# Optimization experiments

Hardware: AMD Instinct MI355X
Metric: run time of the kernel (lower is better)

Reference implementation:

```python
import jax, jax.numpy as jnp
import numpy as np

D = 64
H = 2          # n_heads
HD = D // H    # head_dim = 32
EPS = 1e-5


def _layer_norm(x, gamma, beta):
    mu = jnp.mean(x, axis=-1, keepdims=True)
    var = jnp.var(x, axis=-1, keepdims=True)
    return (x - mu) * jax.lax.rsqrt(var + EPS) * gamma + beta


def setup_inputs() -> dict:
    key = jax.random.key(0)
    ks = jax.random.split(key, 12)
    s = 0.05
    n_stocks, tau = 512, 512
    return {
        "x":     jax.random.normal(ks[0], (n_stocks, tau, D), dtype=jnp.float32),
        "Wqkv":  jax.random.normal(ks[1], (3 * D, D), dtype=jnp.float32) * s,
        "bqkv":  jax.random.normal(ks[2], (3 * D,), dtype=jnp.float32) * s,
        "Wo":    jax.random.normal(ks[3], (D, D), dtype=jnp.float32) * s,
        "bo":    jax.random.normal(ks[4], (D,), dtype=jnp.float32) * s,
        "g1":    jnp.ones((D,), dtype=jnp.float32),
        "beta1": jnp.zeros((D,), dtype=jnp.float32),
        "W1":    jax.random.normal(ks[5], (4 * D, D), dtype=jnp.float32) * s,
        "bf1":   jax.random.normal(ks[6], (4 * D,), dtype=jnp.float32) * s,
        "W2":    jax.random.normal(ks[7], (D, 4 * D), dtype=jnp.float32) * s,
        "bf2":   jax.random.normal(ks[8], (D,), dtype=jnp.float32) * s,
        "g2":    jnp.ones((D,), dtype=jnp.float32),
        "beta2": jnp.zeros((D,), dtype=jnp.float32),
    }


def reference(x, Wqkv, bqkv, Wo, bo, g1, beta1, W1, bf1, W2, bf2, g2, beta2):
    # x: (n_stocks, tau, D). The torch loop over tau == batched attention with
    # batch = tau, seq = n_stocks. Dropout is identity (eval mode).
    n_stocks, tau, d = x.shape
    Ht = jnp.transpose(x, (1, 0, 2))                    # (tau, S, D)

    qkv = Ht @ Wqkv.T + bqkv                            # (tau, S, 3D)
    q, k, v = jnp.split(qkv, 3, axis=-1)
    q = q.reshape(tau, n_stocks, H, HD)
    k = k.reshape(tau, n_stocks, H, HD)
    v = v.reshape(tau, n_stocks, H, HD)

    scores = jnp.einsum("bqhd,bkhd->bhqk", q, k) / jnp.sqrt(jnp.float32(HD))
    attn = jax.nn.softmax(scores, axis=-1)              # (tau, H, S, S)
    ctx = jnp.einsum("bhqk,bkhd->bqhd", attn, v).reshape(tau, n_stocks, D)
    attn_out = ctx @ Wo.T + bo                          # (tau, S, D)

    y = _layer_norm(attn_out + Ht, g1, beta1)           # residual + LN1
    ffn = jax.nn.relu(y @ W1.T + bf1) @ W2.T + bf2      # (tau, S, D)
    z = _layer_norm(ffn + y, g2, beta2)                 # residual + LN2

    return jnp.transpose(z, (1, 0, 2))                  # (n_stocks, tau, D)
```

## Files before the change

### kernel.cpp

```cpp
#include <hip/hip_runtime.h>
#include <hip/hip_bf16.h>
#include <cmath>

#define NS 512
#define NT 512
#define DIM 64
#define HD 32

typedef __attribute__((ext_vector_type(8))) short short8;
typedef __attribute__((ext_vector_type(16))) float f32x16;

union FragU { unsigned w[4]; short8 f; };

__device__ __forceinline__ unsigned short bfbits(float x) {
  __hip_bfloat16 h = __float2bfloat16(x);
  return __builtin_bit_cast(unsigned short, h);
}
__device__ __forceinline__ unsigned pk2(float lo, float hi) {
  return (unsigned)bfbits(lo) | ((unsigned)bfbits(hi) << 16);
}
__device__ __forceinline__ float lo_f(unsigned w) { return __uint_as_float(w << 16); }
__device__ __forceinline__ float hi_f(unsigned w) { return __uint_as_float(w & 0xffff0000u); }
__device__ __forceinline__ short8 ldg8(const __hip_bfloat16* p) {
  return *reinterpret_cast<const short8*>(p);
}

__device__ __forceinline__ void repack(const float* p, int hi, short8& o1, short8& o2) {
  unsigned pk[8], xk[8];
  #pragma unroll
  for (int j = 0; j < 8; ++j) pk[j] = pk2(p[2 * j], p[2 * j + 1]);
  #pragma unroll
  for (int j = 0; j < 8; ++j) xk[j] = (unsigned)__shfl_xor((int)pk[j], 32, 64);
  FragU a1, a2;
  a1.w[0] = hi ? xk[2] : pk[0];
  a1.w[1] = hi ? xk[3] : pk[1];
  a1.w[2] = hi ? pk[2] : xk[0];
  a1.w[3] = hi ? pk[3] : xk[1];
  a2.w[0] = hi ? xk[6] : pk[4];
  a2.w[1] = hi ? xk[7] : pk[5];
  a2.w[2] = hi ? pk[6] : xk[4];
  a2.w[3] = hi ? pk[7] : xk[5];
  o1 = a1.f; o2 = a2.f;
}

__global__ void k_cvt(const float* __restrict__ Wqkv, const float* __restrict__ Wo,
                      const float* __restrict__ W1, const float* __restrict__ W2,
                      __hip_bfloat16* __restrict__ dst) {
  int i = blockIdx.x * 256 + threadIdx.x;
  float v;
  if (i < 12288) v = Wqkv[i];
  else if (i < 16384) v = Wo[i - 12288];
  else if (i < 32768) v = W1[i - 16384];
  else v = W2[i - 32768];
  dst[i] = __float2bfloat16(v);
}

__global__ __launch_bounds__(512, 4) void k_attn(
    const float* __restrict__ x, const __hip_bfloat16* __restrict__ Wb,
    const float* __restrict__ bqkv, __hip_bfloat16* __restrict__ ctx) {
  __shared__ char smem[65536];
  const int t = blockIdx.x, h = blockIdx.y;
  const int tid = threadIdx.x;
  const int l = tid & 63, wv = tid >> 6, hi = l >> 5, l31 = l & 31;

  {
    const float4* xp = reinterpret_cast<const float4*>(x + ((size_t)tid * NT + t) * DIM);
    unsigned xpk[32];
    #pragma unroll
    for (int i = 0; i < 16; ++i) {
      float4 v = xp[i];
      xpk[2 * i]     = pk2(v.x, v.y);
      xpk[2 * i + 1] = pk2(v.z, v.w);
    }
    #pragma unroll
    for (int c = 0; c < 8; ++c) {
      FragU fu;
      fu.w[0] = xpk[4*c]; fu.w[1] = xpk[4*c+1]; fu.w[2] = xpk[4*c+2]; fu.w[3] = xpk[4*c+3];
      *reinterpret_cast<short8*>(smem + tid * 128 + ((c ^ (tid & 7)) << 4)) = fu.f;
    }
  }
  __syncthreads();

  short8 xf[2][4];
  #pragma unroll
  for (int rt = 0; rt < 2; ++rt) {
    int row = wv * 64 + rt * 32 + l31;
    #pragma unroll
    for (int st = 0; st < 4; ++st)
      xf[rt][st] = *reinterpret_cast<const short8*>(
          smem + row * 128 + ((((st << 1) | hi) ^ (row & 7)) << 4));
  }
  __syncthreads();

  short8 qfrag[2][2];
  {
    short8 wqa[4];
    #pragma unroll
    for (int st = 0; st < 4; ++st)
      wqa[st] = ldg8(Wb + (size_t)(h * 32 + l31) * 64 + st * 16 + hi * 8);
    float bqv[16];
    #pragma unroll
    for (int r = 0; r < 16; ++r)
      bqv[r] = bqkv[h * 32 + (r & 3) + 8 * (r >> 2) + 4 * hi];
    #pragma unroll
    for (int rt = 0; rt < 2; ++rt) {
      f32x16 qa = {};
      #pragma unroll
      for (int st = 0; st < 4; ++st)
        qa = __builtin_amdgcn_mfma_f32_32x32x16_bf16(wqa[st], xf[rt][st], qa, 0, 0, 0);
      float p[16];
      #pragma unroll
      for (int r = 0; r < 16; ++r) p[r] = (qa[r] + bqv[r]) * 0.17677669529663687f;
      repack(p, hi, qfrag[rt][0], qfrag[rt][1]);
    }
  }

  {
    short8 wkb[4];
    #pragma unroll
    for (int st = 0; st < 4; ++st)
      wkb[st] = ldg8(Wb + (size_t)(64 + h * 32 + l31) * 64 + st * 16 + hi * 8);
    float bk = bqkv[64 + h * 32 + l31];
    #pragma unroll
    for (int rt = 0; rt < 2; ++rt) {
      f32x16 ka = {};
      #pragma unroll
      for (int st = 0; st < 4; ++st)
        ka = __builtin_amdgcn_mfma_f32_32x32x16_bf16(xf[rt][st], wkb[st], ka, 0, 0, 0);
      #pragma unroll
      for (int r = 0; r < 16; ++r) {
        int key = wv * 64 + rt * 32 + (r & 3) + 8 * (r >> 2) + 4 * hi;
        *reinterpret_cast<unsigned short*>(
            smem + key * 64 + (((l31 >> 3) ^ (key & 3)) << 4) + ((l31 & 7) << 1)) =
            bfbits(ka[r] + bk);
      }
    }
  }

  {
    short8 wvb[4];
    #pragma unroll
    for (int st = 0; st < 4; ++st)
      wvb[st] = ldg8(Wb + (size_t)(128 + h * 32 + l31) * 64 + st * 16 + hi * 8);
    float bv = bqkv[128 + h * 32 + l31];
    #pragma unroll
    for (int rt = 0; rt < 2; ++rt) {
      f32x16 va = {};
      #pragma unroll
      for (int st = 0; st < 4; ++st)
        va = __builtin_amdgcn_mfma_f32_32x32x16_bf16(xf[rt][st], wvb[st], va, 0, 0, 0);
      #pragma unroll
      for (int g = 0; g < 4; ++g) {
        int kb = wv * 64 + rt * 32 + g * 8 + hi * 4;
        uint2 d2 = make_uint2(pk2(va[4*g] + bv, va[4*g+1] + bv),
                              pk2(va[4*g+2] + bv, va[4*g+3] + bv));
        *reinterpret_cast<uint2*>(
            smem + 32768 + l31 * 1024 + ((((kb >> 3) ^ (l31 & 7)) << 4) + ((kb & 7) << 1))) = d2;
      }
    }
  }
  __syncthreads();

  f32x16 oacc[2];
  #pragma unroll
  for (int i = 0; i < 16; ++i) { oacc[0][i] = 0.f; oacc[1][i] = 0.f; }
  float lsum[2] = {0.f, 0.f};

  #pragma clang loop unroll(disable)
  for (int kt = 0; kt < 16; ++kt) {
    short8 kfrag[2], vfrag[2];
    #pragma unroll
    for (int dc = 0; dc < 2; ++dc) {
      int row = kt * 32 + l31;
      kfrag[dc] = *reinterpret_cast<const short8*>(
          smem + row * 64 + ((((dc << 1) | hi) ^ (l31 & 3)) << 4));
    }
    #pragma unroll
    for (int c = 0; c < 2; ++c) {
      int ck = kt * 4 + (c << 1) + hi;
      vfrag[c] = *reinterpret_cast<const short8*>(
          smem + 32768 + l31 * 1024 + ((ck ^ (l31 & 7)) << 4));
    }
    #pragma unroll
    for (int sb = 0; sb < 2; ++sb) {
      f32x16 st = {};
      st = __builtin_amdgcn_mfma_f32_32x32x16_bf16(kfrag[0], qfrag[sb][0], st, 0, 0, 0);
      st = __builtin_amdgcn_mfma_f32_32x32x16_bf16(kfrag[1], qfrag[sb][1], st, 0, 0, 0);
      float p[16];
      #pragma unroll
      for (int r = 0; r < 16; ++r) { p[r] = __expf(st[r]); lsum[sb] += p[r]; }
      short8 a1, a2;
      repack(p, hi, a1, a2);
      oacc[sb] = __builtin_amdgcn_mfma_f32_32x32x16_bf16(a1, vfrag[0], oacc[sb], 0, 0, 0);
      oacc[sb] = __builtin_amdgcn_mfma_f32_32x32x16_bf16(a2, vfrag[1], oacc[sb], 0, 0, 0);
    }
  }

  #pragma unroll
  for (int sb = 0; sb < 2; ++sb) {
    float lt = lsum[sb] + __shfl_xor(lsum[sb], 32, 64);
    float inv = 1.f / lt;
    #pragma unroll
    for (int r = 0; r < 16; ++r) {
      int ql = (r & 3) + 8 * (r >> 2) + 4 * hi;
      float fac = __shfl(inv, ql, 64);
      int q = wv * 64 + sb * 32 + ql;
      ctx[((size_t)t * 512 + q) * 64 + h * 32 + l31] = __float2bfloat16(oacc[sb][r] * fac);
    }
  }
}

__global__ __launch_bounds__(512, 2) void k_tail(
    const __hip_bfloat16* __restrict__ ctx, const float* __restrict__ x,
    const __hip_bfloat16* __restrict__ Wob, const float* __restrict__ bo,
    const float* __restrict__ g1, const float* __restrict__ be1,
    const __hip_bfloat16* __restrict__ W1b, const float* __restrict__ bf1,
    const __hip_bfloat16* __restrict__ W2b, const float* __restrict__ bf2,
    const float* __restrict__ g2, const float* __restrict__ be2,
    float* __restrict__ out) {
  __shared__ char sm[133632];
  float* ps = reinterpret_cast<float*>(sm + 131072);
  const int t = blockIdx.x;
  const int tid = threadIdx.x;
  const int l = tid & 63, wv = tid >> 6, hi = l >> 5, l31 = l & 31;

  {
    const short8* cp = reinterpret_cast<const short8*>(ctx + ((size_t)t * 512 + tid) * 64);
    #pragma unroll
    for (int c = 0; c < 8; ++c)
      *reinterpret_cast<short8*>(sm + tid * 128 + ((c ^ (tid & 7)) << 4)) = cp[c];
  }
  for (int i = tid; i < 640; i += 512) {
    float v;
    if (i < 64) v = g1[i];
    else if (i < 128) v = be1[i - 64];
    else if (i < 192) v = bo[i - 128];
    else if (i < 256) v = bf2[i - 192];
    else if (i < 320) v = g2[i - 256];
    else if (i < 384) v = be2[i - 320];
    else v = bf1[i - 384];
    ps[i] = v;
  }
  __syncthreads();

  {
    short8 cb[2][4];
    #pragma unroll
    for (int stl = 0; stl < 2; ++stl) {
      int row = wv * 64 + stl * 32 + l31;
      #pragma unroll
      for (int st = 0; st < 4; ++st)
        cb[stl][st] = *reinterpret_cast<const short8*>(
            sm + row * 128 + ((((st << 1) | hi) ^ (row & 7)) << 4));
    }
    f32x16 ao[2][2];
    #pragma unroll
    for (int dt = 0; dt < 2; ++dt) {
      short8 wa[4];
      #pragma unroll
      for (int st = 0; st < 4; ++st)
        wa[st] = ldg8(Wob + (size_t)(dt * 32 + l31) * 64 + st * 16 + hi * 8);
      #pragma unroll
      for (int stl = 0; stl < 2; ++stl) {
        f32x16 a = {};
        #pragma unroll
        for (int st = 0; st < 4; ++st)
          a = __builtin_amdgcn_mfma_f32_32x32x16_bf16(wa[st], cb[stl][st], a, 0, 0, 0);
        ao[dt][stl] = a;
      }
    }
    #pragma unroll
    for (int dt = 0; dt < 2; ++dt)
      #pragma unroll
      for (int stl = 0; stl < 2; ++stl) {
        int s_ = wv * 64 + stl * 32 + l31;
        #pragma unroll
        for (int rp = 0; rp < 8; ++rp) {
          int r = 2 * rp;
          int d = dt * 32 + (r & 3) + 8 * (r >> 2) + 4 * hi;
          *reinterpret_cast<unsigned*>(
              sm + s_ * 128 + (((d >> 3) ^ (s_ & 7)) << 4) + ((d & 7) << 1)) =
              pk2(ao[dt][stl][r], ao[dt][stl][r + 1]);
        }
      }
  }
  __syncthreads();

  float y[64];
  {
    float aov[64];
    #pragma unroll
    for (int c = 0; c < 8; ++c) {
      FragU fu;
      fu.f = *reinterpret_cast<const short8*>(sm + tid * 128 + ((c ^ (tid & 7)) << 4));
      #pragma unroll
      for (int u = 0; u < 4; ++u) {
        aov[c * 8 + 2 * u]     = lo_f(fu.w[u]);
        aov[c * 8 + 2 * u + 1] = hi_f(fu.w[u]);
      }
    }
    const float4* xp = reinterpret_cast<const float4*>(x + ((size_t)tid * NT + t) * DIM);
    #pragma unroll
    for (int i = 0; i < 16; ++i) {
      float4 v = xp[i];
      y[4*i+0] = v.x + aov[4*i+0] + ps[128 + 4*i+0];
      y[4*i+1] = v.y + aov[4*i+1] + ps[128 + 4*i+1];
      y[4*i+2] = v.z + aov[4*i+2] + ps[128 + 4*i+2];
      y[4*i+3] = v.w + aov[4*i+3] + ps[128 + 4*i+3];
    }
    float m0 = 0.f, m1 = 0.f, m2 = 0.f, m3 = 0.f;
    #pragma unroll
    for (int j = 0; j < 16; ++j) {
      m0 += y[4*j+0]; m1 += y[4*j+1]; m2 += y[4*j+2]; m3 += y[4*j+3];
    }
    float mu = ((m0 + m1) + (m2 + m3)) * (1.f / 64.f);
    float v0 = 0.f, v1 = 0.f, v2 = 0.f, v3 = 0.f;
    #pragma unroll
    for (int j = 0; j < 16; ++j) {
      float t0 = y[4*j+0] - mu, t1 = y[4*j+1] - mu;
      float t2 = y[4*j+2] - mu, t3 = y[4*j+3] - mu;
      v0 = fmaf(t0, t0, v0); v1 = fmaf(t1, t1, v1);
      v2 = fmaf(t2, t2, v2); v3 = fmaf(t3, t3, v3);
    }
    float var = ((v0 + v1) + (v2 + v3)) * (1.f / 64.f);
    float rs = rsqrtf(var + 1e-5f);
    #pragma unroll
    for (int d = 0; d < 64; ++d) y[d] = (y[d] - mu) * rs * ps[d] + ps[64 + d];
    #pragma unroll
    for (int c = 0; c < 8; ++c) {
      FragU fu;
      #pragma unroll
      for (int u = 0; u < 4; ++u) fu.w[u] = pk2(y[c*8 + 2*u], y[c*8 + 2*u + 1]);
      *reinterpret_cast<short8*>(sm + 65536 + tid * 128 + ((c ^ (tid & 7)) << 4)) = fu.f;
    }
  }
  __syncthreads();

  {
    short8 yb[2][4];
    #pragma unroll
    for (int stl = 0; stl < 2; ++stl) {
      int row = wv * 64 + stl * 32 + l31;
      #pragma unroll
      for (int st = 0; st < 4; ++st)
        yb[stl][st] = *reinterpret_cast<const short8*>(
            sm + 65536 + row * 128 + ((((st << 1) | hi) ^ (row & 7)) << 4));
    }
    f32x16 zacc[2][2];
    #pragma unroll
    for (int i = 0; i < 16; ++i) {
      zacc[0][0][i] = 0.f; zacc[0][1][i] = 0.f; zacc[1][0][i] = 0.f; zacc[1][1][i] = 0.f;
    }
    #pragma clang loop unroll(disable)
    for (int jt = 0; jt < 8; ++jt) {
      short8 w1a[4];
      #pragma unroll
      for (int st = 0; st < 4; ++st)
        w1a[st] = ldg8(W1b + (size_t)(jt * 32 + l31) * 64 + st * 16 + hi * 8);
      short8 w2f[2][2];
      #pragma unroll
      for (int dt = 0; dt < 2; ++dt)
        #pragma unroll
        for (int ks = 0; ks < 2; ++ks)
          w2f[dt][ks] = ldg8(W2b + (size_t)(dt * 32 + l31) * 256 + jt * 32 + ks * 16 + hi * 8);
      float b1v[16];
      #pragma unroll
      for (int r = 0; r < 16; ++r)
        b1v[r] = ps[384 + jt * 32 + (r & 3) + 8 * (r >> 2) + 4 * hi];
      #pragma unroll
      for (int stl = 0; stl < 2; ++stl) {
        f32x16 ha = {};
        #pragma unroll
        for (int st = 0; st < 4; ++st)
          ha = __builtin_amdgcn_mfma_f32_32x32x16_bf16(w1a[st], yb[stl][st], ha, 0, 0, 0);
        float p[16];
        #pragma unroll
        for (int r = 0; r < 16; ++r) p[r] = fmaxf(ha[r] + b1v[r], 0.f);
        short8 b1, b2;
        repack(p, hi, b1, b2);
        zacc[0][stl] = __builtin_amdgcn_mfma_f32_32x32x16_bf16(w2f[0][0], b1, zacc[0][stl], 0, 0, 0);
        zacc[0][stl] = __builtin_amdgcn_mfma_f32_32x32x16_bf16(w2f[0][1], b2, zacc[0][stl], 0, 0, 0);
        zacc[1][stl] = __builtin_amdgcn_mfma_f32_32x32x16_bf16(w2f[1][0], b1, zacc[1][stl], 0, 0, 0);
        zacc[1][stl] = __builtin_amdgcn_mfma_f32_32x32x16_bf16(w2f[1][1], b2, zacc[1][stl], 0, 0, 0);
      }
    }
    #pragma unroll
    for (int dt = 0; dt < 2; ++dt)
      #pragma unroll
      for (int stl = 0; stl < 2; ++stl) {
        int s_ = wv * 64 + stl * 32 + l31;
        #pragma unroll
        for (int rp = 0; rp < 8; ++rp) {
          int r = 2 * rp;
          int d = dt * 32 + (r & 3) + 8 * (r >> 2) + 4 * hi;
          *reinterpret_cast<unsigned*>(
              sm + s_ * 128 + (((d >> 3) ^ (s_ & 7)) << 4) + ((d & 7) << 1)) =
              pk2(zacc[dt][stl][r], zacc[dt][stl][r + 1]);
        }
      }
  }
  __syncthreads();

  {
    float z[64];
    #pragma unroll
    for (int c = 0; c < 8; ++c) {
      FragU zf, yf;
      zf.f = *reinterpret_cast<const short8*>(sm + tid * 128 + ((c ^ (tid & 7)) << 4));
      yf.f = *reinterpret_cast<const short8*>(sm + 65536 + tid * 128 + ((c ^ (tid & 7)) << 4));
      #pragma unroll
      for (int u = 0; u < 4; ++u) {
        int d = c * 8 + 2 * u;
        z[d]     = lo_f(zf.w[u]) + ps[192 + d]     + lo_f(yf.w[u]);
        z[d + 1] = hi_f(zf.w[u]) + ps[192 + d + 1] + hi_f(yf.w[u]);
      }
    }
    float m0 = 0.f, m1 = 0.f, m2 = 0.f, m3 = 0.f;
    #pragma unroll
    for (int j = 0; j < 16; ++j) {
      m0 += z[4*j+0]; m1 += z[4*j+1]; m2 += z[4*j+2]; m3 += z[4*j+3];
    }
    float mu2 = ((m0 + m1) + (m2 + m3)) * (1.f / 64.f);
    float v0 = 0.f, v1 = 0.f, v2 = 0.f, v3 = 0.f;
    #pragma unroll
    for (int j = 0; j < 16; ++j) {
      float t0 = z[4*j+0] - mu2, t1 = z[4*j+1] - mu2;
      float t2 = z[4*j+2] - mu2, t3 = z[4*j+3] - mu2;
      v0 = fmaf(t0, t0, v0); v1 = fmaf(t1, t1, v1);
      v2 = fmaf(t2, t2, v2); v3 = fmaf(t3, t3, v3);
    }
    float var2 = ((v0 + v1) + (v2 + v3)) * (1.f / 64.f);
    float rs2 = rsqrtf(var2 + 1e-5f);
    float4* op = reinterpret_cast<float4*>(out + ((size_t)tid * NT + t) * DIM);
    #pragma unroll
    for (int i = 0; i < 16; ++i) {
      op[i] = make_float4(
          (z[4*i+0] - mu2) * rs2 * ps[256 + 4*i+0] + ps[320 + 4*i+0],
          (z[4*i+1] - mu2) * rs2 * ps[256 + 4*i+1] + ps[320 + 4*i+1],
          (z[4*i+2] - mu2) * rs2 * ps[256 + 4*i+2] + ps[320 + 4*i+2],
          (z[4*i+3] - mu2) * rs2 * ps[256 + 4*i+3] + ps[320 + 4*i+3]);
    }
  }
}

extern "C" void kernel_launch(void* const* d_in, const int* in_sizes, int n_in,
                              void* d_out, int out_size, void* d_ws, size_t ws_size,
                              hipStream_t stream) {
  const float* x    = (const float*)d_in[0];
  const float* Wqkv = (const float*)d_in[1];
  const float* bqkv = (const float*)d_in[2];
  const float* Wo   = (const float*)d_in[3];
  const float* bo   = (const float*)d_in[4];
  const float* g1   = (const float*)d_in[5];
  const float* be1  = (const float*)d_in[6];
  const float* W1   = (const float*)d_in[7];
  const float* bf1  = (const float*)d_in[8];
  const float* W2   = (const float*)d_in[9];
  const float* bf2  = (const float*)d_in[10];
  const float* g2   = (const float*)d_in[11];
  const float* be2  = (const float*)d_in[12];
  float* out = (float*)d_out;

  __hip_bfloat16* wb   = (__hip_bfloat16*)d_ws;
  __hip_bfloat16* ctxb = (__hip_bfloat16*)((char*)d_ws + 131072);

  hipLaunchKernelGGL(k_cvt, dim3(192), dim3(256), 0, stream, Wqkv, Wo, W1, W2, wb);
  hipLaunchKernelGGL(k_attn, dim3(NT, 2), dim3(512), 0, stream, x, wb, bqkv, ctxb);
  hipLaunchKernelGGL(k_tail, dim3(NT), dim3(512), 0, stream,
                     ctxb, x, wb + 12288, bo, g1, be1, wb + 16384, bf1,
                     wb + 32768, bf2, g2, be2, out);
}
```

Baseline: 173.9 us.

## Rework attention and tail kernels: direct x loads, permlane repack, exp2, smaller tail blocks

k_attn now builds its x fragments straight from global memory, which removes an LDS staging pass and two barriers. It replaces shuffle-based repacking with v_permlane32_swap and folds log2(e) into the Q scale so it can use exp2. The K bias is dropped, since it shifts every score of a query by the same amount and cancels in the softmax, and the V bias is applied once at the ctx write. k_tail is split into 256-thread blocks over two stock halves with far less shared memory, keeps y in registers, and writes through transposed MFMA outputs, removing barriers and raising occupancy. The main risks are wave-local LDS reuse without barriers and the changed fragment layouts.

```diff
diff --git a/kernel.cpp b/kernel.cpp
--- a/kernel.cpp
+++ b/kernel.cpp
@@ -12,6 +12,12 @@
 
 union FragU { unsigned w[4]; short8 f; };
 
+#if __has_builtin(__builtin_amdgcn_exp2f)
+#define EXP2F __builtin_amdgcn_exp2f
+#else
+#define EXP2F exp2f
+#endif
+
 __device__ __forceinline__ unsigned short bfbits(float x) {
   __hip_bfloat16 h = __float2bfloat16(x);
   return __builtin_bit_cast(unsigned short, h);
@@ -25,21 +31,21 @@
   return *reinterpret_cast<const short8*>(p);
 }
 
-__device__ __forceinline__ void repack(const float* p, int hi, short8& o1, short8& o2) {
-  unsigned pk[8], xk[8];
+__device__ __forceinline__ void pl32swap(unsigned& a, unsigned& b) {
+  asm volatile("v_permlane32_swap_b32 %0, %1" : "+v"(a), "+v"(b));
+}
+
+__device__ __forceinline__ void repack(const float* p, short8& o1, short8& o2) {
+  unsigned pk[8];
   #pragma unroll
   for (int j = 0; j < 8; ++j) pk[j] = pk2(p[2 * j], p[2 * j + 1]);
-  #pragma unroll
-  for (int j = 0; j < 8; ++j) xk[j] = (unsigned)__shfl_xor((int)pk[j], 32, 64);
+  pl32swap(pk[0], pk[2]);
+  pl32swap(pk[1], pk[3]);
+  pl32swap(pk[4], pk[6]);
+  pl32swap(pk[5], pk[7]);
   FragU a1, a2;
-  a1.w[0] = hi ? xk[2] : pk[0];
-  a1.w[1] = hi ? xk[3] : pk[1];
-  a1.w[2] = hi ? pk[2] : xk[0];
-  a1.w[3] = hi ? pk[3] : xk[1];
-  a2.w[0] = hi ? xk[6] : pk[4];
-  a2.w[1] = hi ? xk[7] : pk[5];
-  a2.w[2] = hi ? pk[6] : xk[4];
-  a2.w[3] = hi ? pk[7] : xk[5];
+  a1.w[0] = pk[0]; a1.w[1] = pk[1]; a1.w[2] = pk[2]; a1.w[3] = pk[3];
+  a2.w[0] = pk[4]; a2.w[1] = pk[5]; a2.w[2] = pk[6]; a2.w[3] = pk[7];
   o1 = a1.f; o2 = a2.f;
 }
 
@@ -63,34 +69,65 @@
   const int tid = threadIdx.x;
   const int l = tid & 63, wv = tid >> 6, hi = l >> 5, l31 = l & 31;
 
-  {
-    const float4* xp = reinterpret_cast<const float4*>(x + ((size_t)tid * NT + t) * DIM);
-    unsigned xpk[32];
-    #pragma unroll
-    for (int i = 0; i < 16; ++i) {
-      float4 v = xp[i];
-      xpk[2 * i]     = pk2(v.x, v.y);
-      xpk[2 * i + 1] = pk2(v.z, v.w);
-    }
-    #pragma unroll
-    for (int c = 0; c < 8; ++c) {
-      FragU fu;
-      fu.w[0] = xpk[4*c]; fu.w[1] = xpk[4*c+1]; fu.w[2] = xpk[4*c+2]; fu.w[3] = xpk[4*c+3];
-      *reinterpret_cast<short8*>(smem + tid * 128 + ((c ^ (tid & 7)) << 4)) = fu.f;
-    }
-  }
-  __syncthreads();
-
   short8 xf[2][4];
   #pragma unroll
   for (int rt = 0; rt < 2; ++rt) {
     int row = wv * 64 + rt * 32 + l31;
+    const float* xr = x + ((size_t)row * NT + t) * DIM + hi * 8;
+    #pragma unroll
+    for (int st = 0; st < 4; ++st) {
+      float4 f0 = *reinterpret_cast<const float4*>(xr + st * 16);
+      float4 f1 = *reinterpret_cast<const float4*>(xr + st * 16 + 4);
+      FragU fu;
+      fu.w[0] = pk2(f0.x, f0.y); fu.w[1] = pk2(f0.z, f0.w);
+      fu.w[2] = pk2(f1.x, f1.y); fu.w[3] = pk2(f1.z, f1.w);
+      xf[rt][st] = fu.f;
+    }
+  }
+
+  {
+    short8 wkb[4];
     #pragma unroll
     for (int st = 0; st < 4; ++st)
-      xf[rt][st] = *reinterpret_cast<const short8*>(
-          smem + row * 128 + ((((st << 1) | hi) ^ (row & 7)) << 4));
-  }
-  __syncthreads();
+      wkb[st] = ldg8(Wb + (size_t)(64 + h * 32 + l31) * 64 + st * 16 + hi * 8);
+    #pragma unroll
+    for (int rt = 0; rt < 2; ++rt) {
+      f32x16 ka = {};
+      #pragma unroll
+      for (int st = 0; st < 4; ++st)
+        ka = __builtin_amdgcn_mfma_f32_32x32x16_bf16(wkb[st], xf[rt][st], ka, 0, 0, 0);
+      int stock = wv * 64 + rt * 32 + l31;
+      char* kb = smem + stock * 64 + (hi << 3);
+      #pragma unroll
+      for (int rq = 0; rq < 4; ++rq) {
+        uint2 d2 = make_uint2(pk2(ka[4 * rq + 0], ka[4 * rq + 1]),
+                              pk2(ka[4 * rq + 2], ka[4 * rq + 3]));
+        *reinterpret_cast<uint2*>(kb + ((rq ^ ((stock >> 1) & 3)) << 4)) = d2;
+      }
+    }
+  }
+
+  {
+    short8 wvb[4];
+    #pragma unroll
+    for (int st = 0; st < 4; ++st)
+      wvb[st] = ldg8(Wb + (size_t)(128 + h * 32 + l31) * 64 + st * 16 + hi * 8);
+    #pragma unroll
+    for (int rt = 0; rt < 2; ++rt) {
+      f32x16 va = {};
+      #pragma unroll
+      for (int st = 0; st < 4; ++st)
+        va = __builtin_amdgcn_mfma_f32_32x32x16_bf16(xf[rt][st], wvb[st], va, 0, 0, 0);
+      #pragma unroll
+      for (int g = 0; g < 4; ++g) {
+        int kb = wv * 64 + rt * 32 + g * 8 + hi * 4;
+        uint2 d2 = make_uint2(pk2(va[4 * g + 0], va[4 * g + 1]),
+                              pk2(va[4 * g + 2], va[4 * g + 3]));
+        *reinterpret_cast<uint2*>(
+            smem + 32768 + l31 * 1024 + (((kb >> 3) ^ (l31 & 7)) << 4) + ((kb & 7) << 1)) = d2;
+      }
+    }
+  }
 
   short8 qfrag[2][2];
   {
@@ -110,55 +147,16 @@
         qa = __builtin_amdgcn_mfma_f32_32x32x16_bf16(wqa[st], xf[rt][st], qa, 0, 0, 0);
       float p[16];
       #pragma unroll
-      for (int r = 0; r < 16; ++r) p[r] = (qa[r] + bqv[r]) * 0.17677669529663687f;
-      repack(p, hi, qfrag[rt][0], qfrag[rt][1]);
-    }
-  }
-
-  {
-    short8 wkb[4];
-    #pragma unroll
-    for (int st = 0; st < 4; ++st)
-      wkb[st] = ldg8(Wb + (size_t)(64 + h * 32 + l31) * 64 + st * 16 + hi * 8);
-    float bk = bqkv[64 + h * 32 + l31];
-    #pragma unroll
-    for (int rt = 0; rt < 2; ++rt) {
-      f32x16 ka = {};
-      #pragma unroll
-      for (int st = 0; st < 4; ++st)
-        ka = __builtin_amdgcn_mfma_f32_32x32x16_bf16(xf[rt][st], wkb[st], ka, 0, 0, 0);
-      #pragma unroll
-      for (int r = 0; r < 16; ++r) {
-        int key = wv * 64 + rt * 32 + (r & 3) + 8 * (r >> 2) + 4 * hi;
-        *reinterpret_cast<unsigned short*>(
-            smem + key * 64 + (((l31 >> 3) ^ (key & 3)) << 4) + ((l31 & 7) << 1)) =
-            bfbits(ka[r] + bk);
-      }
-    }
-  }
-
-  {
-    short8 wvb[4];
-    #pragma unroll
-    for (int st = 0; st < 4; ++st)
-      wvb[st] = ldg8(Wb + (size_t)(128 + h * 32 + l31) * 64 + st * 16 + hi * 8);
-    float bv = bqkv[128 + h * 32 + l31];
-    #pragma unroll
-    for (int rt = 0; rt < 2; ++rt) {
-      f32x16 va = {};
-      #pragma unroll
-      for (int st = 0; st < 4; ++st)
-        va = __builtin_amdgcn_mfma_f32_32x32x16_bf16(xf[rt][st], wvb[st], va, 0, 0, 0);
-      #pragma unroll
-      for (int g = 0; g < 4; ++g) {
-        int kb = wv * 64 + rt * 32 + g * 8 + hi * 4;
-        uint2 d2 = make_uint2(pk2(va[4*g] + bv, va[4*g+1] + bv),
-                              pk2(va[4*g+2] + bv, va[4*g+3] + bv));
-        *reinterpret_cast<uint2*>(
-            smem + 32768 + l31 * 1024 + ((((kb >> 3) ^ (l31 & 7)) << 4) + ((kb & 7) << 1))) = d2;
-      }
-    }
-  }
+      for (int r = 0; r < 16; ++r) p[r] = (qa[r] + bqv[r]) * 0.25503488921708395f;
+      repack(p, qfrag[rt][0], qfrag[rt][1]);
+    }
+  }
+
+  float bvv[16];
+  #pragma unroll
+  for (int r = 0; r < 16; ++r)
+    bvv[r] = bqkv[128 + h * 32 + (r & 3) + 8 * (r >> 2) + 4 * hi];
+
   __syncthreads();
 
   f32x16 oacc[2];
@@ -169,12 +167,11 @@
   #pragma clang loop unroll(disable)
   for (int kt = 0; kt < 16; ++kt) {
     short8 kfrag[2], vfrag[2];
-    #pragma unroll
-    for (int dc = 0; dc < 2; ++dc) {
-      int row = kt * 32 + l31;
+    int row = kt * 32 + l31;
+    #pragma unroll
+    for (int dc = 0; dc < 2; ++dc)
       kfrag[dc] = *reinterpret_cast<const short8*>(
-          smem + row * 64 + ((((dc << 1) | hi) ^ (l31 & 3)) << 4));
-    }
+          smem + row * 64 + ((((dc << 1) | hi) ^ ((row >> 1) & 3)) << 4));
     #pragma unroll
     for (int c = 0; c < 2; ++c) {
       int ck = kt * 4 + (c << 1) + hi;
@@ -183,16 +180,16 @@
     }
     #pragma unroll
     for (int sb = 0; sb < 2; ++sb) {
-      f32x16 st = {};
-      st = __builtin_amdgcn_mfma_f32_32x32x16_bf16(kfrag[0], qfrag[sb][0], st, 0, 0, 0);
-      st = __builtin_amdgcn_mfma_f32_32x32x16_bf16(kfrag[1], qfrag[sb][1], st, 0, 0, 0);
+      f32x16 sC = {};
+      sC = __builtin_amdgcn_mfma_f32_32x32x16_bf16(kfrag[0], qfrag[sb][0], sC, 0, 0, 0);
+      sC = __builtin_amdgcn_mfma_f32_32x32x16_bf16(kfrag[1], qfrag[sb][1], sC, 0, 0, 0);
       float p[16];
       #pragma unroll
-      for (int r = 0; r < 16; ++r) { p[r] = __expf(st[r]); lsum[sb] += p[r]; }
+      for (int r = 0; r < 16; ++r) { p[r] = EXP2F(sC[r]); lsum[sb] += p[r]; }
       short8 a1, a2;
-      repack(p, hi, a1, a2);
-      oacc[sb] = __builtin_amdgcn_mfma_f32_32x32x16_bf16(a1, vfrag[0], oacc[sb], 0, 0, 0);
-      oacc[sb] = __builtin_amdgcn_mfma_f32_32x32x16_bf16(a2, vfrag[1], oacc[sb], 0, 0, 0);
+      repack(p, a1, a2);
+      oacc[sb] = __builtin_amdgcn_mfma_f32_32x32x16_bf16(vfrag[0], a1, oacc[sb], 0, 0, 0);
+      oacc[sb] = __builtin_amdgcn_mfma_f32_32x32x16_bf16(vfrag[1], a2, oacc[sb], 0, 0, 0);
     }
   }
 
@@ -200,37 +197,42 @@
   for (int sb = 0; sb < 2; ++sb) {
     float lt = lsum[sb] + __shfl_xor(lsum[sb], 32, 64);
     float inv = 1.f / lt;
-    #pragma unroll
-    for (int r = 0; r < 16; ++r) {
-      int ql = (r & 3) + 8 * (r >> 2) + 4 * hi;
-      float fac = __shfl(inv, ql, 64);
-      int q = wv * 64 + sb * 32 + ql;
-      ctx[((size_t)t * 512 + q) * 64 + h * 32 + l31] = __float2bfloat16(oacc[sb][r] * fac);
-    }
-  }
-}
-
-__global__ __launch_bounds__(512, 2) void k_tail(
+    int q = wv * 64 + sb * 32 + l31;
+    __hip_bfloat16* cb = ctx + ((size_t)t * 512 + q) * 64 + h * 32;
+    #pragma unroll
+    for (int g = 0; g < 4; ++g) {
+      uint2 d2 = make_uint2(
+          pk2(fmaf(oacc[sb][4 * g + 0], inv, bvv[4 * g + 0]),
+              fmaf(oacc[sb][4 * g + 1], inv, bvv[4 * g + 1])),
+          pk2(fmaf(oacc[sb][4 * g + 2], inv, bvv[4 * g + 2]),
+              fmaf(oacc[sb][4 * g + 3], inv, bvv[4 * g + 3])));
+      *reinterpret_cast<uint2*>(cb + 8 * g + 4 * hi) = d2;
+    }
+  }
+}
+
+__global__ __launch_bounds__(256, 2) void k_tail(
     const __hip_bfloat16* __restrict__ ctx, const float* __restrict__ x,
-    const __hip_bfloat16* __restrict__ Wob, const float* __restrict__ bo,
-    const float* __restrict__ g1, const float* __restrict__ be1,
-    const __hip_bfloat16* __restrict__ W1b, const float* __restrict__ bf1,
-    const __hip_bfloat16* __restrict__ W2b, const float* __restrict__ bf2,
-    const float* __restrict__ g2, const float* __restrict__ be2,
-    float* __restrict__ out) {
-  __shared__ char sm[133632];
-  float* ps = reinterpret_cast<float*>(sm + 131072);
-  const int t = blockIdx.x;
+    const __hip_bfloat16* __restrict__ Wob,
+    const float* __restrict__ bo, const float* __restrict__ g1,
+    const float* __restrict__ be1, const __hip_bfloat16* __restrict__ W1b,
+    const float* __restrict__ bf1, const __hip_bfloat16* __restrict__ W2b,
+    const float* __restrict__ bf2, const float* __restrict__ g2,
+    const float* __restrict__ be2, float* __restrict__ out) {
+  __shared__ char sm[35328];
+  float* ps = reinterpret_cast<float*>(sm + 32768);
+  const int t = blockIdx.y;
   const int tid = threadIdx.x;
+  const int s = blockIdx.x * 256 + tid;
   const int l = tid & 63, wv = tid >> 6, hi = l >> 5, l31 = l & 31;
 
   {
-    const short8* cp = reinterpret_cast<const short8*>(ctx + ((size_t)t * 512 + tid) * 64);
+    const short8* cp = reinterpret_cast<const short8*>(ctx + ((size_t)t * 512 + s) * 64);
     #pragma unroll
     for (int c = 0; c < 8; ++c)
       *reinterpret_cast<short8*>(sm + tid * 128 + ((c ^ (tid & 7)) << 4)) = cp[c];
   }
-  for (int i = tid; i < 640; i += 512) {
+  for (int i = tid; i < 640; i += 256) {
     float v;
     if (i < 64) v = g1[i];
     else if (i < 128) v = be1[i - 64];
@@ -247,13 +249,12 @@
     short8 cb[2][4];
     #pragma unroll
     for (int stl = 0; stl < 2; ++stl) {
-      int row = wv * 64 + stl * 32 + l31;
+      int lr = wv * 64 + stl * 32 + l31;
       #pragma unroll
       for (int st = 0; st < 4; ++st)
         cb[stl][st] = *reinterpret_cast<const short8*>(
-            sm + row * 128 + ((((st << 1) | hi) ^ (row & 7)) << 4));
-    }
-    f32x16 ao[2][2];
+            sm + lr * 128 + ((((st << 1) | hi) ^ (lr & 7)) << 4));
+    }
     #pragma unroll
     for (int dt = 0; dt < 2; ++dt) {
       short8 wa[4];
@@ -266,47 +267,40 @@
         #pragma unroll
         for (int st = 0; st < 4; ++st)
           a = __builtin_amdgcn_mfma_f32_32x32x16_bf16(wa[st], cb[stl][st], a, 0, 0, 0);
-        ao[dt][stl] = a;
-      }
-    }
-    #pragma unroll
-    for (int dt = 0; dt < 2; ++dt)
-      #pragma unroll
-      for (int stl = 0; stl < 2; ++stl) {
-        int s_ = wv * 64 + stl * 32 + l31;
+        int lr = wv * 64 + stl * 32 + l31;
         #pragma unroll
-        for (int rp = 0; rp < 8; ++rp) {
-          int r = 2 * rp;
-          int d = dt * 32 + (r & 3) + 8 * (r >> 2) + 4 * hi;
-          *reinterpret_cast<unsigned*>(
-              sm + s_ * 128 + (((d >> 3) ^ (s_ & 7)) << 4) + ((d & 7) << 1)) =
-              pk2(ao[dt][stl][r], ao[dt][stl][r + 1]);
+        for (int q = 0; q < 4; ++q) {
+          uint2 d2 = make_uint2(pk2(a[4 * q + 0], a[4 * q + 1]),
+                                pk2(a[4 * q + 2], a[4 * q + 3]));
+          *reinterpret_cast<uint2*>(
+              sm + lr * 128 + (((dt * 4 + q) ^ (lr & 7)) << 4) + (hi << 3)) = d2;
         }
       }
-  }
-  __syncthreads();
-
-  float y[64];
-  {
-    float aov[64];
+    }
+  }
+
+  unsigned ypk[32];
+  {
+    float ao[64];
     #pragma unroll
     for (int c = 0; c < 8; ++c) {
       FragU fu;
       fu.f = *reinterpret_cast<const short8*>(sm + tid * 128 + ((c ^ (tid & 7)) << 4));
       #pragma unroll
       for (int u = 0; u < 4; ++u) {
-        aov[c * 8 + 2 * u]     = lo_f(fu.w[u]);
-        aov[c * 8 + 2 * u + 1] = hi_f(fu.w[u]);
-      }
-    }
-    const float4* xp = reinterpret_cast<const float4*>(x + ((size_t)tid * NT + t) * DIM);
+        ao[c * 8 + 2 * u]     = lo_f(fu.w[u]);
+        ao[c * 8 + 2 * u + 1] = hi_f(fu.w[u]);
+      }
+    }
+    float y[64];
+    const float4* xp = reinterpret_cast<const float4*>(x + ((size_t)s * NT + t) * DIM);
     #pragma unroll
     for (int i = 0; i < 16; ++i) {
       float4 v = xp[i];
-      y[4*i+0] = v.x + aov[4*i+0] + ps[128 + 4*i+0];
-      y[4*i+1] = v.y + aov[4*i+1] + ps[128 + 4*i+1];
-      y[4*i+2] = v.z + aov[4*i+2] + ps[128 + 4*i+2];
-      y[4*i+3] = v.w + aov[4*i+3] + ps[128 + 4*i+3];
+      y[4*i+0] = v.x + ao[4*i+0] + ps[128 + 4*i+0];
+      y[4*i+1] = v.y + ao[4*i+1] + ps[128 + 4*i+1];
+      y[4*i+2] = v.z + ao[4*i+2] + ps[128 + 4*i+2];
+      y[4*i+3] = v.w + ao[4*i+3] + ps[128 + 4*i+3];
     }
     float m0 = 0.f, m1 = 0.f, m2 = 0.f, m3 = 0.f;
     #pragma unroll
@@ -330,27 +324,25 @@
     for (int c = 0; c < 8; ++c) {
       FragU fu;
       #pragma unroll
-      for (int u = 0; u < 4; ++u) fu.w[u] = pk2(y[c*8 + 2*u], y[c*8 + 2*u + 1]);
-      *reinterpret_cast<short8*>(sm + 65536 + tid * 128 + ((c ^ (tid & 7)) << 4)) = fu.f;
-    }
-  }
-  __syncthreads();
-
-  {
-    short8 yb[2][4];
-    #pragma unroll
-    for (int stl = 0; stl < 2; ++stl) {
-      int row = wv * 64 + stl * 32 + l31;
-      #pragma unroll
-      for (int st = 0; st < 4; ++st)
-        yb[stl][st] = *reinterpret_cast<const short8*>(
-            sm + 65536 + row * 128 + ((((st << 1) | hi) ^ (row & 7)) << 4));
-    }
-    f32x16 zacc[2][2];
-    #pragma unroll
-    for (int i = 0; i < 16; ++i) {
-      zacc[0][0][i] = 0.f; zacc[0][1][i] = 0.f; zacc[1][0][i] = 0.f; zacc[1][1][i] = 0.f;
-    }
+      for (int u = 0; u < 4; ++u) {
+        fu.w[u] = pk2(y[c*8 + 2*u], y[c*8 + 2*u + 1]);
+        ypk[4 * c + u] = fu.w[u];
+      }
+      *reinterpret_cast<short8*>(sm + tid * 128 + ((c ^ (tid & 7)) << 4)) = fu.f;
+    }
+  }
+
+  #pragma unroll
+  for (int stl = 0; stl < 2; ++stl) {
+    int lr = wv * 64 + stl * 32 + l31;
+    short8 yb[4];
+    #pragma unroll
+    for (int st = 0; st < 4; ++st)
+      yb[st] = *reinterpret_cast<const short8*>(
+          sm + lr * 128 + ((((st << 1) | hi) ^ (lr & 7)) << 4));
+    f32x16 zacc[2];
+    #pragma unroll
+    for (int i = 0; i < 16; ++i) { zacc[0][i] = 0.f; zacc[1][i] = 0.f; }
     #pragma clang loop unroll(disable)
     for (int jt = 0; jt < 8; ++jt) {
       short8 w1a[4];
@@ -367,52 +359,42 @@
       #pragma unroll
       for (int r = 0; r < 16; ++r)
         b1v[r] = ps[384 + jt * 32 + (r & 3) + 8 * (r >> 2) + 4 * hi];
-      #pragma unroll
-      for (int stl = 0; stl < 2; ++stl) {
-        f32x16 ha = {};
-        #pragma unroll
-        for (int st = 0; st < 4; ++st)
-          ha = __builtin_amdgcn_mfma_f32_32x32x16_bf16(w1a[st], yb[stl][st], ha, 0, 0, 0);
-        float p[16];
-        #pragma unroll
-        for (int r = 0; r < 16; ++r) p[r] = fmaxf(ha[r] + b1v[r], 0.f);
-        short8 b1, b2;
-        repack(p, hi, b1, b2);
-        zacc[0][stl] = __builtin_amdgcn_mfma_f32_32x32x16_bf16(w2f[0][0], b1, zacc[0][stl], 0, 0, 0);
-        zacc[0][stl] = __builtin_amdgcn_mfma_f32_32x32x16_bf16(w2f[0][1], b2, zacc[0][stl], 0, 0, 0);
-        zacc[1][stl] = __builtin_amdgcn_mfma_f32_32x32x16_bf16(w2f[1][0], b1, zacc[1][stl], 0, 0, 0);
-        zacc[1][stl] = __builtin_amdgcn_mfma_f32_32x32x16_bf16(w2f[1][1], b2, zacc[1][stl], 0, 0, 0);
-      }
+      f32x16 ha = {};
+      #pragma unroll
+      for (int st = 0; st < 4; ++st)
+        ha = __builtin_amdgcn_mfma_f32_32x32x16_bf16(w1a[st], yb[st], ha, 0, 0, 0);
+      float p[16];
+      #pragma unroll
+      for (int r = 0; r < 16; ++r) p[r] = fmaxf(ha[r] + b1v[r], 0.f);
+      short8 b1, b2;
+      repack(p, b1, b2);
+      zacc[0] = __builtin_amdgcn_mfma_f32_32x32x16_bf16(w2f[0][0], b1, zacc[0], 0, 0, 0);
+      zacc[0] = __builtin_amdgcn_mfma_f32_32x32x16_bf16(w2f[0][1], b2, zacc[0], 0, 0, 0);
+      zacc[1] = __builtin_amdgcn_mfma_f32_32x32x16_bf16(w2f[1][0], b1, zacc[1], 0, 0, 0);
+      zacc[1] = __builtin_amdgcn_mfma_f32_32x32x16_bf16(w2f[1][1], b2, zacc[1], 0, 0, 0);
     }
     #pragma unroll
     for (int dt = 0; dt < 2; ++dt)
       #pragma unroll
-      for (int stl = 0; stl < 2; ++stl) {
-        int s_ = wv * 64 + stl * 32 + l31;
-        #pragma unroll
-        for (int rp = 0; rp < 8; ++rp) {
-          int r = 2 * rp;
-          int d = dt * 32 + (r & 3) + 8 * (r >> 2) + 4 * hi;
-          *reinterpret_cast<unsigned*>(
-              sm + s_ * 128 + (((d >> 3) ^ (s_ & 7)) << 4) + ((d & 7) << 1)) =
-              pk2(zacc[dt][stl][r], zacc[dt][stl][r + 1]);
-        }
-      }
-  }
-  __syncthreads();
+      for (int q = 0; q < 4; ++q) {
+        uint2 d2 = make_uint2(pk2(zacc[dt][4 * q + 0], zacc[dt][4 * q + 1]),
+                              pk2(zacc[dt][4 * q + 2], zacc[dt][4 * q + 3]));
+        *reinterpret_cast<uint2*>(
+            sm + lr * 128 + (((dt * 4 + q) ^ (lr & 7)) << 4) + (hi << 3)) = d2;
+      }
+  }
 
   {
     float z[64];
     #pragma unroll
     for (int c = 0; c < 8; ++c) {
-      FragU zf, yf;
+      FragU zf;
       zf.f = *reinterpret_cast<const short8*>(sm + tid * 128 + ((c ^ (tid & 7)) << 4));
-      yf.f = *reinterpret_cast<const short8*>(sm + 65536 + tid * 128 + ((c ^ (tid & 7)) << 4));
       #pragma unroll
       for (int u = 0; u < 4; ++u) {
         int d = c * 8 + 2 * u;
-        z[d]     = lo_f(zf.w[u]) + ps[192 + d]     + lo_f(yf.w[u]);
-        z[d + 1] = hi_f(zf.w[u]) + ps[192 + d + 1] + hi_f(yf.w[u]);
+        z[d]     = lo_f(zf.w[u]) + ps[192 + d]     + lo_f(ypk[4 * c + u]);
+        z[d + 1] = hi_f(zf.w[u]) + ps[192 + d + 1] + hi_f(ypk[4 * c + u]);
       }
     }
     float m0 = 0.f, m1 = 0.f, m2 = 0.f, m3 = 0.f;
@@ -431,7 +413,7 @@
     }
     float var2 = ((v0 + v1) + (v2 + v3)) * (1.f / 64.f);
     float rs2 = rsqrtf(var2 + 1e-5f);
-    float4* op = reinterpret_cast<float4*>(out + ((size_t)tid * NT + t) * DIM);
+    float4* op = reinterpret_cast<float4*>(out + ((size_t)s * NT + t) * DIM);
     #pragma unroll
     for (int i = 0; i < 16; ++i) {
       op[i] = make_float4(
@@ -466,7 +448,7 @@
 
   hipLaunchKernelGGL(k_cvt, dim3(192), dim3(256), 0, stream, Wqkv, Wo, W1, W2, wb);
   hipLaunchKernelGGL(k_attn, dim3(NT, 2), dim3(512), 0, stream, x, wb, bqkv, ctxb);
-  hipLaunchKernelGGL(k_tail, dim3(NT), dim3(512), 0, stream,
+  hipLaunchKernelGGL(k_tail, dim3(2, NT), dim3(256), 0, stream,
                      ctxb, x, wb + 12288, bo, g1, be1, wb + 16384, bf1,
                      wb + 32768, bf2, g2, be2, out);
 }
```

Measured after the change: 184.4 us. +6.1%, slower.
